# Optimization experiments

Measured on AMD Instinct MI355X. Metric: run time of the kernel, lower is better.

## Reference

```python
import jax, jax.numpy as jnp
import numpy as np

NHEAD = 16
EPS = 1e-5

def layer_norm(x, g, b):
    mu = jnp.mean(x, axis=-1, keepdims=True)
    var = jnp.mean(jnp.square(x - mu), axis=-1, keepdims=True)
    return (x - mu) * jax.lax.rsqrt(var + EPS) * g + b

def setup_inputs() -> dict:
    key = jax.random.key(0)
    ks = jax.random.split(key, 12)
    d_model, d_hid = 1024, 4096  # MHA num_hiddens == dim_feedforward (source quirk)
    B, S = 2, 2048
    s_in = 1.0 / np.sqrt(d_model)
    s_hid = 1.0 / np.sqrt(d_hid)
    return {
        "x": jax.random.normal(ks[0], (B, S, d_model), jnp.float32),
        "Wq": jax.random.normal(ks[1], (d_model, d_hid), jnp.float32) * s_in,
        "Wk": jax.random.normal(ks[2], (d_model, d_hid), jnp.float32) * s_in,
        "Wv": jax.random.normal(ks[3], (d_model, d_hid), jnp.float32) * s_in,
        "Wo": jax.random.normal(ks[4], (d_hid, d_model), jnp.float32) * s_hid,
        "W1": jax.random.normal(ks[5], (d_model, d_hid), jnp.float32) * s_in,
        "b1": jnp.zeros((d_hid,), jnp.float32),
        "W2": jax.random.normal(ks[6], (d_hid, d_model), jnp.float32) * s_hid,
        "b2": jnp.zeros((d_model,), jnp.float32),
        "g1": jnp.ones((d_model,), jnp.float32),
        "be1": jnp.zeros((d_model,), jnp.float32),
        "g2": jnp.ones((d_model,), jnp.float32),
        "be2": jnp.zeros((d_model,), jnp.float32),
    }

def reference(x, Wq, Wk, Wv, Wo, W1, b1, W2, b2, g1, be1, g2, be2):
    B, S, D = x.shape
    H = NHEAD
    # pre-norm attention branch (dropout = identity at eval)
    x1 = layer_norm(x, g1, be1)
    q = (x1 @ Wq).reshape(B, S, H, -1)  # [B,S,H,dh], dh = num_hiddens/H
    k = (x1 @ Wk).reshape(B, S, H, -1)
    v = (x1 @ Wv).reshape(B, S, H, -1)
    dh = q.shape[-1]
    scores = jnp.einsum('bqhd,bkhd->bhqk', q, k) / jnp.sqrt(jnp.float32(dh))
    attn = jax.nn.softmax(scores, axis=-1)
    ctx = jnp.einsum('bhqk,bkhd->bqhd', attn, v).reshape(B, S, -1)
    x = x + ctx @ Wo
    # pre-norm FFN branch
    x2 = layer_norm(x, g2, be2)
    h = jax.nn.relu(x2 @ W1 + b1)
    out = x + (h @ W2 + b2)
    return out
```

## Files before the change

### kernel.cpp

```cpp
#include <hip/hip_runtime.h>
#include <hip/hip_bf16.h>
#include <stdint.h>

using bf16x8 = __attribute__((ext_vector_type(8))) __bf16;
using f32x4  = __attribute__((ext_vector_type(4))) float;

__device__ __forceinline__ uint16_t f2bf(float f) {
    uint32_t u = __builtin_bit_cast(uint32_t, f);
    u += 0x7FFFu + ((u >> 16) & 1u);
    return (uint16_t)(u >> 16);
}
__device__ __forceinline__ uint32_t pack2bf(float lo, float hi) {
    return (uint32_t)f2bf(lo) | ((uint32_t)f2bf(hi) << 16);
}

__device__ __forceinline__ void gld_lds16(const void* g, void* l) {
    __builtin_amdgcn_global_load_lds(
        (const __attribute__((address_space(1))) void*)g,
        (__attribute__((address_space(3))) void*)l,
        16, 0, 0);
}

__global__ __launch_bounds__(256)
void wconvB(const float* __restrict__ i0, const float* __restrict__ i1,
            const float* __restrict__ i2, uint16_t* __restrict__ o0,
            uint16_t* __restrict__ o1, uint16_t* __restrict__ o2,
            int R, int C) {
    int z = blockIdx.z;
    const float* in = z == 0 ? i0 : (z == 1 ? i1 : i2);
    uint16_t* out   = z == 0 ? o0 : (z == 1 ? o1 : o2);
    __shared__ float t[32][33];
    int c0 = blockIdx.x * 32, r0 = blockIdx.y * 32;
    int tx = threadIdx.x & 31, ty = threadIdx.x >> 5;
    #pragma unroll
    for (int i = 0; i < 32; i += 8)
        t[ty + i][tx] = in[(size_t)(r0 + ty + i) * C + c0 + tx];
    __syncthreads();
    #pragma unroll
    for (int i = 0; i < 32; i += 8)
        out[(size_t)(c0 + ty + i) * R + r0 + tx] = f2bf(t[tx][ty + i]);
}

__global__ __launch_bounds__(256)
void ln_bf16(const float* __restrict__ x, const float* __restrict__ gw,
             const float* __restrict__ bw, uint16_t* __restrict__ out) {
    const int D = 1024;
    int row = blockIdx.x;
    float4 v = ((const float4*)(x + (size_t)row * D))[threadIdx.x];
    float s  = v.x + v.y + v.z + v.w;
    float ss = v.x * v.x + v.y * v.y + v.z * v.z + v.w * v.w;
    #pragma unroll
    for (int m = 1; m < 64; m <<= 1) {
        s  += __shfl_xor(s, m);
        ss += __shfl_xor(ss, m);
    }
    __shared__ float red[8];
    int wid = threadIdx.x >> 6, lane = threadIdx.x & 63;
    if (lane == 0) { red[wid] = s; red[4 + wid] = ss; }
    __syncthreads();
    s  = red[0] + red[1] + red[2] + red[3];
    ss = red[4] + red[5] + red[6] + red[7];
    float mu  = s * (1.f / 1024.f);
    float var = ss * (1.f / 1024.f) - mu * mu;
    float rstd = rsqrtf(var + 1e-5f);
    float4 gv = ((const float4*)gw)[threadIdx.x];
    float4 bv = ((const float4*)bw)[threadIdx.x];
    ushort4 o;
    o.x = f2bf((v.x - mu) * rstd * gv.x + bv.x);
    o.y = f2bf((v.y - mu) * rstd * gv.y + bv.y);
    o.z = f2bf((v.z - mu) * rstd * gv.z + bv.z);
    o.w = f2bf((v.w - mu) * rstd * gv.w + bv.w);
    ((ushort4*)(out + (size_t)row * D))[threadIdx.x] = o;
}

template <int EPI>
__global__ __launch_bounds__(256, 2)
void gemm128p(const uint16_t* __restrict__ A, const uint16_t* __restrict__ B,
              float* __restrict__ Cf, const float* __restrict__ bias,
              const float* __restrict__ resid, int M, int N, int K) {
    __shared__ uint8_t smem[65536];
    int bid = blockIdx.x;
    int cpx = gridDim.x >> 3;
    bid = (bid & 7) * cpx + (bid >> 3);
    int nbn  = N >> 7;
    int brow = (bid / nbn) << 7;
    int bcol = (bid % nbn) << 7;
    int t0 = threadIdx.x;
    int wid = t0 >> 6, lane = t0 & 63;
    int wr = wid >> 1, wc = wid & 1;
    int q = lane & 15, g = lane >> 4;

    const uint16_t* Asw = A + (size_t)(brow + (lane >> 3)) * K + (((lane & 7) ^ (lane >> 3)) << 3);
    const uint16_t* Bsw = B + (size_t)(bcol + (lane >> 3)) * K + (((lane & 7) ^ (lane >> 3)) << 3);

    f32x4 acc[4][4] = {};
    int NKT = K >> 6;

#define STG128(BSEL, KK)                                                       \
    {                                                                          \
        uint8_t* dA = smem + (BSEL) * 16384;                                   \
        uint8_t* dB = smem + 32768 + (BSEL) * 16384;                           \
        _Pragma("unroll")                                                      \
        for (int i = 0; i < 4; ++i) {                                          \
            int c = wid * 4 + i;                                               \
            gld_lds16(Asw + (size_t)(c * 8) * K + (KK), dA + c * 1024);        \
            gld_lds16(Bsw + (size_t)(c * 8) * K + (KK), dB + c * 1024);        \
        }                                                                      \
    }

    STG128(0, 0)

    for (int t = 0; t < NKT; ++t) {
        int cur = t & 1;
        if (t + 1 < NKT) {
            STG128(cur ^ 1, (t + 1) << 6)
            asm volatile("s_waitcnt vmcnt(8)" ::: "memory");
        } else {
            asm volatile("s_waitcnt vmcnt(0)" ::: "memory");
        }
        __builtin_amdgcn_sched_barrier(0);
        __builtin_amdgcn_s_barrier();
        __builtin_amdgcn_sched_barrier(0);

        const uint8_t* bA = smem + cur * 16384;
        const uint8_t* bB = smem + 32768 + cur * 16384;

        bf16x8 af[4][2], bfr[4][2];
        #pragma unroll
        for (int m2 = 0; m2 < 4; ++m2)
            #pragma unroll
            for (int ks = 0; ks < 2; ++ks) {
                int rr = wr * 64 + m2 * 16 + q;
                int sl = (ks * 4 + g) ^ (q & 7);
                af[m2][ks] = *(const bf16x8*)(bA + rr * 128 + sl * 16);
            }
        #pragma unroll
        for (int n2 = 0; n2 < 4; ++n2)
            #pragma unroll
            for (int ks = 0; ks < 2; ++ks) {
                int cc = wc * 64 + n2 * 16 + q;
                int sl = (ks * 4 + g) ^ (q & 7);
                bfr[n2][ks] = *(const bf16x8*)(bB + cc * 128 + sl * 16);
            }
        __builtin_amdgcn_s_setprio(1);
        #pragma unroll
        for (int m2 = 0; m2 < 4; ++m2)
            #pragma unroll
            for (int n2 = 0; n2 < 4; ++n2)
                #pragma unroll
                for (int ks = 0; ks < 2; ++ks)
                    acc[m2][n2] = __builtin_amdgcn_mfma_f32_16x16x32_bf16(
                        af[m2][ks], bfr[n2][ks], acc[m2][n2], 0, 0, 0);
        __builtin_amdgcn_s_setprio(0);
        __builtin_amdgcn_s_barrier();
    }

    #pragma unroll
    for (int m2 = 0; m2 < 4; ++m2)
        #pragma unroll
        for (int n2 = 0; n2 < 4; ++n2)
            #pragma unroll
            for (int r = 0; r < 4; ++r) {
                int gr = brow + wr * 64 + m2 * 16 + g * 4 + r;
                int gc = bcol + wc * 64 + n2 * 16 + q;
                float v = acc[m2][n2][r];
                size_t idx = (size_t)gr * N + gc;
                if constexpr (EPI == 2) {
                    Cf[idx] = v + bias[gc] + resid[idx];
                } else {
                    Cf[idx] = v + resid[idx];
                }
            }
#undef STG128
}

template <int EPI>
__global__ __launch_bounds__(512, 2)
void gemm256(const uint16_t* __restrict__ A, const uint16_t* __restrict__ B,
             void* __restrict__ Cp, const float* __restrict__ bias,
             int M, int N, int K) {
    __shared__ uint8_t smem[131072];
    int bid = blockIdx.x;
    int cpx = gridDim.x >> 3;
    bid = (bid & 7) * cpx + (bid >> 3);
    int nbn  = N >> 8;
    int brow = (bid / nbn) << 8;
    int bcol = (bid % nbn) << 8;
    int t0 = threadIdx.x;
    int wid = t0 >> 6, lane = t0 & 63;
    int wr = wid >> 2, wc = wid & 3;
    int q = lane & 15, g = lane >> 4;

    const uint16_t* Asw = A + (size_t)(brow + (lane >> 3)) * K + (((lane & 7) ^ (lane >> 3)) << 3);
    const uint16_t* Bsw = B + (size_t)(bcol + (lane >> 3)) * K + (((lane & 7) ^ (lane >> 3)) << 3);

    f32x4 acc[2][2][4][2] = {};
    int NKT = K >> 6;

#define STAGE256(BSEL, KK)                                                     \
    {                                                                          \
        uint8_t* dA = smem + (BSEL) * 32768;                                   \
        uint8_t* dB = smem + 65536 + (BSEL) * 32768;                           \
        _Pragma("unroll")                                                      \
        for (int i = 0; i < 4; ++i) {                                          \
            int c = wid * 4 + i;                                               \
            gld_lds16(Asw + (size_t)(c * 8) * K + (KK), dA + c * 1024);        \
            gld_lds16(Bsw + (size_t)(c * 8) * K + (KK), dB + c * 1024);        \
        }                                                                      \
    }

    STAGE256(0, 0)

    for (int t = 0; t < NKT; ++t) {
        int cur = t & 1;
        if (t + 1 < NKT) {
            STAGE256(cur ^ 1, (t + 1) << 6)
            asm volatile("s_waitcnt vmcnt(8)" ::: "memory");
        } else {
            asm volatile("s_waitcnt vmcnt(0)" ::: "memory");
        }
        __builtin_amdgcn_sched_barrier(0);
        __builtin_amdgcn_s_barrier();
        __builtin_amdgcn_sched_barrier(0);

        const uint8_t* bA = smem + cur * 32768;
        const uint8_t* bB = smem + 65536 + cur * 32768;

        bf16x8 af[4][2], bfr[2][2];

#define LOADA256(MH)                                                           \
        _Pragma("unroll")                                                      \
        for (int m2 = 0; m2 < 4; ++m2)                                         \
            _Pragma("unroll")                                                  \
            for (int ks = 0; ks < 2; ++ks) {                                   \
                int rr = wr * 128 + (MH) * 64 + m2 * 16 + q;                   \
                int sl = (ks * 4 + g) ^ (q & 7);                               \
                af[m2][ks] = *(const bf16x8*)(bA + rr * 128 + sl * 16);        \
            }
#define LOADB256(NH)                                                           \
        _Pragma("unroll")                                                      \
        for (int n2 = 0; n2 < 2; ++n2)                                         \
            _Pragma("unroll")                                                  \
            for (int ks = 0; ks < 2; ++ks) {                                   \
                int cc = wc * 64 + (NH) * 32 + n2 * 16 + q;                    \
                int sl = (ks * 4 + g) ^ (q & 7);                               \
                bfr[n2][ks] = *(const bf16x8*)(bB + cc * 128 + sl * 16);       \
            }
#define MMQ256(MH, NH)                                                         \
        __builtin_amdgcn_s_setprio(1);                                         \
        _Pragma("unroll")                                                      \
        for (int m2 = 0; m2 < 4; ++m2)                                         \
            _Pragma("unroll")                                                  \
            for (int n2 = 0; n2 < 2; ++n2)                                     \
                _Pragma("unroll")                                              \
                for (int ks = 0; ks < 2; ++ks)                                 \
                    acc[MH][NH][m2][n2] = __builtin_amdgcn_mfma_f32_16x16x32_bf16( \
                        af[m2][ks], bfr[n2][ks], acc[MH][NH][m2][n2], 0, 0, 0);\
        __builtin_amdgcn_s_setprio(0);

        LOADA256(0) LOADB256(0) MMQ256(0, 0)
        LOADB256(1) MMQ256(0, 1)
        LOADA256(1) MMQ256(1, 1)
        LOADB256(0) MMQ256(1, 0)

        __builtin_amdgcn_s_barrier();
    }

    uint16_t* Cb = (uint16_t*)Cp;
    #pragma unroll
    for (int mh = 0; mh < 2; ++mh)
        #pragma unroll
        for (int nh = 0; nh < 2; ++nh)
            #pragma unroll
            for (int m2 = 0; m2 < 4; ++m2)
                #pragma unroll
                for (int n2 = 0; n2 < 2; ++n2)
                    #pragma unroll
                    for (int r = 0; r < 4; ++r) {
                        int gr = brow + wr * 128 + mh * 64 + m2 * 16 + g * 4 + r;
                        int gc = bcol + wc * 64 + nh * 32 + n2 * 16 + q;
                        float v = acc[mh][nh][m2][n2][r];
                        if constexpr (EPI == 1) {
                            v += bias[gc];
                            v = v > 0.f ? v : 0.f;
                        }
                        Cb[(size_t)gr * N + gc] = f2bf(v);
                    }
#undef STAGE256
#undef LOADA256
#undef LOADB256
#undef MMQ256
}

__device__ __forceinline__ void attn_stage(uint8_t* smem, int bufsel,
        const uint16_t* Kb0, const uint16_t* Vb0, int ktok, int wid, int lane) {
    #pragma unroll
    for (int i = 0; i < 4; ++i) {
        int chunk = wid * 4 + i;
        int r = 2 * chunk + (lane >> 5);
        int s = lane & 31;
        int cg = (s & ~7) | ((s ^ r) & 7);
        gld_lds16(Kb0 + (size_t)(ktok + r) * 8192 + cg * 8,
                  smem + bufsel * 16384 + chunk * 1024);
    }
    #pragma unroll
    for (int i = 0; i < 4; ++i) {
        int chunk = wid * 4 + i;
        int r = 16 * chunk + (lane >> 2);
        int s = lane & 3;
        int cg = s ^ (r & 3);
        gld_lds16(Vb0 + (size_t)r * 4096 + ktok + cg * 8,
                  smem + 32768 + bufsel * 16384 + chunk * 1024);
    }
}

__device__ __forceinline__ bf16x8 sm_pack(const f32x4* sacc, f32x4* acc,
                                          float& m_run, float& l_run,
                                          int q, int g) {
    float mx = fmaxf(fmaxf(fmaxf(sacc[0][0], sacc[0][1]), fmaxf(sacc[0][2], sacc[0][3])),
                     fmaxf(fmaxf(sacc[1][0], sacc[1][1]), fmaxf(sacc[1][2], sacc[1][3])));
    mx = fmaxf(mx, __shfl_xor(mx, 16));
    mx = fmaxf(mx, __shfl_xor(mx, 32));
    if (!__all(mx - m_run <= 8.f)) {
        float m_new = fmaxf(m_run, mx);
        float alpha = __expf(m_run - m_new);
        l_run *= alpha;
        #pragma unroll
        for (int td = 0; td < 16; ++td) {
            acc[td][0] *= alpha; acc[td][1] *= alpha;
            acc[td][2] *= alpha; acc[td][3] *= alpha;
        }
        m_run = m_new;
    }
    float p[8]; float rs = 0.f;
    #pragma unroll
    for (int tm = 0; tm < 2; ++tm)
        #pragma unroll
        for (int r = 0; r < 4; ++r) {
            float e = __expf(sacc[tm][r] - m_run);
            p[tm * 4 + r] = e; rs += e;
        }
    l_run += rs;

    uint32_t pk0 = pack2bf(p[0], p[1]);
    uint32_t pk1 = pack2bf(p[2], p[3]);
    uint32_t pk2 = pack2bf(p[4], p[5]);
    uint32_t pk3 = pack2bf(p[6], p[7]);
    int srcA = ((g & 1) << 5) + q;
    int srcB = srcA + 16;
    uint32_t a0 = __shfl(pk0, srcA), a1 = __shfl(pk2, srcA);
    uint32_t b0 = __shfl(pk1, srcA), b1 = __shfl(pk3, srcA);
    uint32_t c0 = __shfl(pk0, srcB), c1 = __shfl(pk2, srcB);
    uint32_t d0 = __shfl(pk1, srcB), d1 = __shfl(pk3, srcB);
    bool hi = g >= 2;
    uint4 pb;
    pb.x = hi ? a1 : a0;
    pb.y = hi ? b1 : b0;
    pb.z = hi ? c1 : c0;
    pb.w = hi ? d1 : d0;
    return __builtin_bit_cast(bf16x8, pb);
}

__global__ __launch_bounds__(256, 2)
void attn(const uint16_t* __restrict__ Qg, const uint16_t* __restrict__ Kg,
          const uint16_t* __restrict__ Vtg, uint16_t* __restrict__ Og) {
    const int S = 2048, NT = 64, QKS = 8192, OC = 4096;
    __shared__ uint8_t smem[65536];

    int id = blockIdx.x;
    id = (id & 7) * 64 + (id >> 3);
    int qb = id & 15, h = (id >> 4) & 15, b = id >> 8;

    int t = threadIdx.x;
    int wid = t >> 6, lane = t & 63;
    int q = lane & 15, g = lane >> 4;
    int tok0 = b * S + qb * 128 + wid * 32;

    bf16x8 qf0[8], qf1[8];
    {
        const uint16_t* qrow0 = Qg + (size_t)(tok0 + q) * QKS + h * 256 + g * 8;
        const uint16_t* qrow1 = Qg + (size_t)(tok0 + 16 + q) * QKS + h * 256 + g * 8;
        #pragma unroll
        for (int c = 0; c < 8; ++c) {
            bf16x8 r0 = *(const bf16x8*)(qrow0 + c * 32);
            bf16x8 r1 = *(const bf16x8*)(qrow1 + c * 32);
            #pragma unroll
            for (int i = 0; i < 8; ++i) {
                r0[i] = (__bf16)((float)r0[i] * 0.0625f);
                r1[i] = (__bf16)((float)r1[i] * 0.0625f);
            }
            qf0[c] = r0; qf1[c] = r1;
        }
    }

    f32x4 acc0[16] = {}, acc1[16] = {};
    float m0 = -1e30f, l0 = 0.f;
    float m1 = -1e30f, l1 = 0.f;

    const uint16_t* Kb0 = Kg + (size_t)(b * S) * QKS + h * 256;
    const uint16_t* Vb0 = Vtg + (size_t)(h * 256) * 4096 + b * S;

    attn_stage(smem, 0, Kb0, Vb0, 0, wid, lane);

    for (int kt = 0; kt < NT; ++kt) {
        int cb = (kt & 1) * 16384;
        if (kt + 1 < NT) {
            attn_stage(smem, (kt + 1) & 1, Kb0, Vb0, (kt + 1) * 32, wid, lane);
            asm volatile("s_waitcnt vmcnt(8)" ::: "memory");
        } else {
            asm volatile("s_waitcnt vmcnt(0)" ::: "memory");
        }
        __builtin_amdgcn_sched_barrier(0);
        __builtin_amdgcn_s_barrier();

        const uint16_t* sk = (const uint16_t*)(smem + cb);
        const uint16_t* sv = (const uint16_t*)(smem + 32768 + cb);

        f32x4 sA0[2] = {}, sA1[2] = {};
        __builtin_amdgcn_s_setprio(1);
        #pragma unroll
        for (int c = 0; c < 8; ++c) {
            #pragma unroll
            for (int tm = 0; tm < 2; ++tm) {
                int G = c * 4 + g;
                int slot = (G & ~7) | ((G ^ q) & 7);
                bf16x8 kf = *(const bf16x8*)(sk + (tm * 16 + q) * 256 + slot * 8);
                sA0[tm] = __builtin_amdgcn_mfma_f32_16x16x32_bf16(kf, qf0[c], sA0[tm], 0, 0, 0);
                sA1[tm] = __builtin_amdgcn_mfma_f32_16x16x32_bf16(kf, qf1[c], sA1[tm], 0, 0, 0);
            }
        }
        __builtin_amdgcn_s_setprio(0);

        bf16x8 pfrag0 = sm_pack(sA0, acc0, m0, l0, q, g);
        bf16x8 pfrag1 = sm_pack(sA1, acc1, m1, l1, q, g);

        int sl = g ^ (q & 3);
        __builtin_amdgcn_s_setprio(1);
        #pragma unroll
        for (int td = 0; td < 16; ++td) {
            bf16x8 vf = *(const bf16x8*)(sv + (td * 16 + q) * 32 + sl * 8);
            acc0[td] = __builtin_amdgcn_mfma_f32_16x16x32_bf16(vf, pfrag0, acc0[td], 0, 0, 0);
            acc1[td] = __builtin_amdgcn_mfma_f32_16x16x32_bf16(vf, pfrag1, acc1[td], 0, 0, 0);
        }
        __builtin_amdgcn_s_setprio(0);
        __builtin_amdgcn_s_barrier();
    }

    l0 += __shfl_xor(l0, 16); l0 += __shfl_xor(l0, 32);
    l1 += __shfl_xor(l1, 16); l1 += __shfl_xor(l1, 32);

    __syncthreads();
    {
        float inv0 = 1.f / l0, inv1 = 1.f / l1;
        uint32_t* w0 = (uint32_t*)(smem + wid * 16384);
        uint32_t* w1 = (uint32_t*)(smem + wid * 16384 + 8192);
        #pragma unroll
        for (int td = 0; td < 16; ++td) {
            int base = (q * 256 + td * 16 + g * 4) >> 1;
            w0[base]     = pack2bf(acc0[td][0] * inv0, acc0[td][1] * inv0);
            w0[base + 1] = pack2bf(acc0[td][2] * inv0, acc0[td][3] * inv0);
            w1[base]     = pack2bf(acc1[td][0] * inv1, acc1[td][1] * inv1);
            w1[base + 1] = pack2bf(acc1[td][2] * inv1, acc1[td][3] * inv1);
        }
    }
    __syncthreads();
    #pragma unroll
    for (int s2 = 0; s2 < 2; ++s2) {
        const uint16_t* tb = (const uint16_t*)(smem + wid * 16384 + s2 * 8192);
        #pragma unroll
        for (int r2 = 0; r2 < 8; ++r2) {
            int c = r2 * 64 + lane;
            int qq = c >> 5, dc = c & 31;
            uint4 v = *(const uint4*)&tb[qq * 256 + dc * 8];
            *(uint4*)(Og + (size_t)(tok0 + s2 * 16 + qq) * OC + h * 256 + dc * 8) = v;
        }
    }
}

extern "C" void kernel_launch(void* const* d_in, const int* in_sizes, int n_in,
                              void* d_out, int out_size, void* d_ws, size_t ws_size,
                              hipStream_t stream) {
    const float* x   = (const float*)d_in[0];
    const float* Wq  = (const float*)d_in[1];
    const float* Wk  = (const float*)d_in[2];
    const float* Wv  = (const float*)d_in[3];
    const float* Wo  = (const float*)d_in[4];
    const float* W1  = (const float*)d_in[5];
    const float* b1  = (const float*)d_in[6];
    const float* W2  = (const float*)d_in[7];
    const float* b2  = (const float*)d_in[8];
    const float* g1  = (const float*)d_in[9];
    const float* be1 = (const float*)d_in[10];
    const float* g2  = (const float*)d_in[11];
    const float* be2 = (const float*)d_in[12];

    char* ws = (char*)d_ws;
    const size_t M8 = 8388608;
    uint16_t* WqkT = (uint16_t*)(ws + 0 * M8);
    uint16_t* WqT  = WqkT;
    uint16_t* WkT  = (uint16_t*)(ws + 1 * M8);
    uint16_t* WvT  = (uint16_t*)(ws + 2 * M8);
    uint16_t* WoT  = (uint16_t*)(ws + 3 * M8);
    uint16_t* W1T  = (uint16_t*)(ws + 4 * M8);
    uint16_t* W2T  = (uint16_t*)(ws + 5 * M8);
    uint16_t* x1   = (uint16_t*)(ws + 6 * M8);
    uint16_t* x2   = (uint16_t*)(ws + 7 * M8);
    uint16_t* QK   = (uint16_t*)(ws + 8 * M8);
    uint16_t* Vt   = (uint16_t*)(ws + 16 * M8);
    uint16_t* ctx  = (uint16_t*)(ws + 20 * M8);
    float*    xmid = (float*)(ws + 12 * M8);
    uint16_t* Hn   = (uint16_t*)(ws + 8 * M8);

    wconvB<<<dim3(128, 32, 3), 256, 0, stream>>>(Wq, Wk, Wv, WqT, WkT, WvT, 1024, 4096);
    wconvB<<<dim3(32, 128, 2), 256, 0, stream>>>(Wo, W2, nullptr, WoT, W2T, nullptr, 4096, 1024);
    wconvB<<<dim3(128, 32, 1), 256, 0, stream>>>(W1, nullptr, nullptr, W1T, nullptr, nullptr, 1024, 4096);

    ln_bf16<<<4096, 256, 0, stream>>>(x, g1, be1, x1);

    gemm256<0><<<512, 512, 0, stream>>>(x1, WqkT, QK, nullptr, 4096, 8192, 1024);
    gemm256<0><<<256, 512, 0, stream>>>(WvT, x1, Vt, nullptr, 4096, 4096, 1024);

    attn<<<512, 256, 0, stream>>>(QK, QK + 4096, Vt, ctx);

    gemm128p<3><<<256, 256, 0, stream>>>(ctx, WoT, xmid, nullptr, x, 4096, 1024, 4096);

    ln_bf16<<<4096, 256, 0, stream>>>(xmid, g2, be2, x2);

    gemm256<1><<<256, 512, 0, stream>>>(x2, W1T, Hn, b1, 4096, 4096, 1024);
    gemm128p<2><<<256, 256, 0, stream>>>(Hn, W2T, (float*)d_out, b2, xmid, 4096, 1024, 4096);
}
```

Baseline: 453.3 us.

## Restructure 256x256 GEMM into half-tile staged pipeline with interleaved loads

Splits the A and B tiles of the 256x256 bf16 GEMM into 128-row halves, each with its own LDS slot. Global-to-LDS loads for the next k-tile are issued at fine granularity between the eight MFMA quadrant steps of a two-k-tile unrolled loop. The warp-to-output mapping changes so each quadrant covers contiguous 128x128 regions, and the epilogue indexing is updated to match. The aim is better overlap of memory traffic with MFMA work. The cost is many more barriers and lgkmcnt waits per iteration, and the loop assumes an even number of k-tiles.

```diff
diff --git a/kernel.cpp b/kernel.cpp
--- a/kernel.cpp
+++ b/kernel.cpp
@@ -195,101 +195,123 @@
     const uint16_t* Bsw = B + (size_t)(bcol + (lane >> 3)) * K + (((lane & 7) ^ (lane >> 3)) << 3);
 
     f32x4 acc[2][2][4][2] = {};
+    bf16x8 af[4][2], bfr[2][2];
     int NKT = K >> 6;
 
-#define STAGE256(BSEL, KK)                                                     \
+#define STGA(P, H, T)                                                          \
     {                                                                          \
-        uint8_t* dA = smem + (BSEL) * 32768;                                   \
-        uint8_t* dB = smem + 65536 + (BSEL) * 32768;                           \
+        uint8_t* d = smem + (((P) * 2 + (H)) << 14);                           \
         _Pragma("unroll")                                                      \
-        for (int i = 0; i < 4; ++i) {                                          \
-            int c = wid * 4 + i;                                               \
-            gld_lds16(Asw + (size_t)(c * 8) * K + (KK), dA + c * 1024);        \
-            gld_lds16(Bsw + (size_t)(c * 8) * K + (KK), dB + c * 1024);        \
+        for (int i = 0; i < 2; ++i) {                                          \
+            int c = wid * 2 + i;                                               \
+            gld_lds16(Asw + (size_t)((H) * 128 + c * 8) * K + ((T) << 6),      \
+                      d + c * 1024);                                           \
         }                                                                      \
     }
-
-    STAGE256(0, 0)
-
-    for (int t = 0; t < NKT; ++t) {
-        int cur = t & 1;
-        if (t + 1 < NKT) {
-            STAGE256(cur ^ 1, (t + 1) << 6)
-            asm volatile("s_waitcnt vmcnt(8)" ::: "memory");
-        } else {
-            asm volatile("s_waitcnt vmcnt(0)" ::: "memory");
-        }
-        __builtin_amdgcn_sched_barrier(0);
-        __builtin_amdgcn_s_barrier();
-        __builtin_amdgcn_sched_barrier(0);
-
-        const uint8_t* bA = smem + cur * 32768;
-        const uint8_t* bB = smem + 65536 + cur * 32768;
-
-        bf16x8 af[4][2], bfr[2][2];
-
-#define LOADA256(MH)                                                           \
+#define STGB(P, H, T)                                                          \
+    {                                                                          \
+        uint8_t* d = smem + 65536 + (((P) * 2 + (H)) << 14);                   \
+        _Pragma("unroll")                                                      \
+        for (int i = 0; i < 2; ++i) {                                          \
+            int c = wid * 2 + i;                                               \
+            gld_lds16(Bsw + (size_t)((H) * 128 + c * 8) * K + ((T) << 6),      \
+                      d + c * 1024);                                           \
+        }                                                                      \
+    }
+#define RDA(P, MQ)                                                             \
+    {                                                                          \
+        const uint8_t* bA = smem + (((P) * 2 + (MQ)) << 14);                   \
         _Pragma("unroll")                                                      \
         for (int m2 = 0; m2 < 4; ++m2)                                         \
             _Pragma("unroll")                                                  \
-            for (int ks = 0; ks < 2; ++ks) {                                   \
-                int rr = wr * 128 + (MH) * 64 + m2 * 16 + q;                   \
-                int sl = (ks * 4 + g) ^ (q & 7);                               \
-                af[m2][ks] = *(const bf16x8*)(bA + rr * 128 + sl * 16);        \
-            }
-#define LOADB256(NH)                                                           \
+            for (int ks = 0; ks < 2; ++ks)                                     \
+                af[m2][ks] = *(const bf16x8*)(bA + (wr * 64 + m2 * 16 + q) * 128 \
+                                              + (((ks * 4 + g) ^ (q & 7)) << 4)); \
+    }
+#define RDB(P, NQ)                                                             \
+    {                                                                          \
+        const uint8_t* bB = smem + 65536 + (((P) * 2 + (NQ)) << 14);           \
         _Pragma("unroll")                                                      \
         for (int n2 = 0; n2 < 2; ++n2)                                         \
             _Pragma("unroll")                                                  \
-            for (int ks = 0; ks < 2; ++ks) {                                   \
-                int cc = wc * 64 + (NH) * 32 + n2 * 16 + q;                    \
-                int sl = (ks * 4 + g) ^ (q & 7);                               \
-                bfr[n2][ks] = *(const bf16x8*)(bB + cc * 128 + sl * 16);       \
-            }
-#define MMQ256(MH, NH)                                                         \
-        __builtin_amdgcn_s_setprio(1);                                         \
+            for (int ks = 0; ks < 2; ++ks)                                     \
+                bfr[n2][ks] = *(const bf16x8*)(bB + (wc * 32 + n2 * 16 + q) * 128 \
+                                               + (((ks * 4 + g) ^ (q & 7)) << 4)); \
+    }
+#define BARR  __builtin_amdgcn_s_barrier();
+#define LGKM0 asm volatile("s_waitcnt lgkmcnt(0)" ::: "memory");
+#define VM4   asm volatile("s_waitcnt vmcnt(4)" ::: "memory");
+#define VM0   asm volatile("s_waitcnt vmcnt(0)" ::: "memory");
+#define MM(MQ, NQ)                                                             \
+    __builtin_amdgcn_s_setprio(1);                                             \
+    _Pragma("unroll")                                                          \
+    for (int m2 = 0; m2 < 4; ++m2)                                             \
         _Pragma("unroll")                                                      \
-        for (int m2 = 0; m2 < 4; ++m2)                                         \
+        for (int n2 = 0; n2 < 2; ++n2)                                         \
             _Pragma("unroll")                                                  \
-            for (int n2 = 0; n2 < 2; ++n2)                                     \
-                _Pragma("unroll")                                              \
-                for (int ks = 0; ks < 2; ++ks)                                 \
-                    acc[MH][NH][m2][n2] = __builtin_amdgcn_mfma_f32_16x16x32_bf16( \
-                        af[m2][ks], bfr[n2][ks], acc[MH][NH][m2][n2], 0, 0, 0);\
-        __builtin_amdgcn_s_setprio(0);
-
-        LOADA256(0) LOADB256(0) MMQ256(0, 0)
-        LOADB256(1) MMQ256(0, 1)
-        LOADA256(1) MMQ256(1, 1)
-        LOADB256(0) MMQ256(1, 0)
-
-        __builtin_amdgcn_s_barrier();
+            for (int ks = 0; ks < 2; ++ks)                                     \
+                acc[MQ][NQ][m2][n2] = __builtin_amdgcn_mfma_f32_16x16x32_bf16( \
+                    af[m2][ks], bfr[n2][ks], acc[MQ][NQ][m2][n2], 0, 0, 0);    \
+    __builtin_amdgcn_s_setprio(0);
+
+    STGA(0, 0, 0) STGB(0, 1, 0) STGB(0, 0, 0) STGA(0, 1, 0)
+    STGA(1, 0, 1) STGB(1, 1, 1)
+    VM4
+    BARR
+
+    int NIT = NKT >> 1;
+    for (int it = 0; it < NIT; ++it) {
+        int t = it << 1;
+        bool nl = (t + 2) < NKT;
+        RDA(0, 0) RDB(0, 0) STGB(1, 0, t + 1)
+        BARR LGKM0 MM(0, 0) BARR
+        RDB(0, 1) STGA(1, 1, t + 1)
+        BARR LGKM0 MM(0, 1) BARR
+        RDA(0, 1) if (nl) { STGA(0, 0, t + 2) }
+        BARR LGKM0 MM(1, 1) BARR
+        RDB(0, 0)
+        if (nl) { STGB(0, 1, t + 2) VM4 } else { VM0 }
+        BARR LGKM0 MM(1, 0) BARR
+        RDA(1, 0) RDB(1, 0) if (nl) { STGB(0, 0, t + 2) }
+        BARR LGKM0 MM(0, 0) BARR
+        RDB(1, 1) if (nl) { STGA(0, 1, t + 2) }
+        BARR LGKM0 MM(0, 1) BARR
+        RDA(1, 1) if (nl) { STGA(1, 0, t + 3) }
+        BARR LGKM0 MM(1, 1) BARR
+        RDB(1, 0)
+        if (nl) { STGB(1, 1, t + 3) VM4 }
+        BARR LGKM0 MM(1, 0) BARR
     }
 
     uint16_t* Cb = (uint16_t*)Cp;
     #pragma unroll
-    for (int mh = 0; mh < 2; ++mh)
-        #pragma unroll
-        for (int nh = 0; nh < 2; ++nh)
+    for (int mq = 0; mq < 2; ++mq)
+        #pragma unroll
+        for (int nq = 0; nq < 2; ++nq)
             #pragma unroll
             for (int m2 = 0; m2 < 4; ++m2)
                 #pragma unroll
                 for (int n2 = 0; n2 < 2; ++n2)
                     #pragma unroll
                     for (int r = 0; r < 4; ++r) {
-                        int gr = brow + wr * 128 + mh * 64 + m2 * 16 + g * 4 + r;
-                        int gc = bcol + wc * 64 + nh * 32 + n2 * 16 + q;
-                        float v = acc[mh][nh][m2][n2][r];
+                        int gr = brow + mq * 128 + wr * 64 + m2 * 16 + g * 4 + r;
+                        int gc = bcol + nq * 128 + wc * 32 + n2 * 16 + q;
+                        float v = acc[mq][nq][m2][n2][r];
                         if constexpr (EPI == 1) {
                             v += bias[gc];
                             v = v > 0.f ? v : 0.f;
                         }
                         Cb[(size_t)gr * N + gc] = f2bf(v);
                     }
-#undef STAGE256
-#undef LOADA256
-#undef LOADB256
-#undef MMQ256
+#undef STGA
+#undef STGB
+#undef RDA
+#undef RDB
+#undef BARR
+#undef LGKM0
+#undef VM4
+#undef VM0
+#undef MM
 }
 
 __device__ __forceinline__ void attn_stage(uint8_t* smem, int bufsel,
```

Result: slower. 463.0 us (+2.1%).
